# Performance work log

Measured on AMD Instinct MI355X. Metric: run time of the kernel, lower is better.

The kernel has to match this reference:

```python
import jax, jax.numpy as jnp
import numpy as np

N, E = 100000, 1600000
NFEAT, NHID, NCLASS, NLAYER = 128, 128, 40, 3


def _glorot(key, shape):
    fan_in, fan_out = shape[0], shape[1]
    lim = float(np.sqrt(6.0 / (fan_in + fan_out)))
    return jax.random.uniform(key, shape, jnp.float32, -lim, lim)


def setup_inputs() -> dict:
    key = jax.random.key(0)
    ks = jax.random.split(key, 12)
    x = jax.random.normal(ks[0], (N, NFEAT), jnp.float32)
    src = jax.random.randint(ks[1], (E,), 0, N, jnp.int32)
    dst = jax.random.randint(ks[2], (E,), 0, N, jnp.int32)
    W1 = _glorot(ks[3], (NFEAT, NHID)); b1 = jnp.zeros((NHID,), jnp.float32)
    W2 = _glorot(ks[4], (NHID, NHID)); b2 = jnp.zeros((NHID,), jnp.float32)
    Wg = jnp.stack([_glorot(ks[5 + l], (NHID, NHID)) for l in range(NLAYER)])  # [L,H,H]
    bg = jnp.zeros((NLAYER, NHID), jnp.float32)
    Wc = _glorot(ks[5 + NLAYER], (NHID, NCLASS)); bc = jnp.zeros((NCLASS,), jnp.float32)
    return {"x": x, "src": src, "dst": dst, "W1": W1, "b1": b1, "W2": W2,
            "b2": b2, "Wg": Wg, "bg": bg, "Wc": Wc, "bc": bc}


def _graph_conv(h, src, dst, W, b, out_norm, in_norm):
    # DGL GraphConv norm='both': scale by src out-deg^{-1/2}, sum-aggregate,
    # scale by dst in-deg^{-1/2}, then linear (in_feats == out_feats -> W after agg).
    h = h * out_norm[:, None]
    agg = jax.ops.segment_sum(h[src], dst, num_segments=N)
    return (agg * in_norm[:, None]) @ W + b


def reference(x, src, dst, W1, b1, W2, b2, Wg, bg, Wc, bc):
    ones = jnp.ones((E,), jnp.float32)
    out_deg = jnp.clip(jax.ops.segment_sum(ones, src, num_segments=N), 1.0)
    in_deg = jnp.clip(jax.ops.segment_sum(ones, dst, num_segments=N), 1.0)
    out_norm = jax.lax.rsqrt(out_deg)
    in_norm = jax.lax.rsqrt(in_deg)

    h = x @ W1 + b1            # feature1
    h = h @ W2 + b2            # feature2
    for l in range(NLAYER):    # stacked GraphConv + ReLU (dropout is identity in eval)
        h = _graph_conv(h, src, dst, Wg[l], bg[l], out_norm, in_norm)
        h = jax.nn.relu(h)
    return h @ Wc + bc         # classifier
```

## Files before the change

### kernel.cpp

```cpp
#include <hip/hip_runtime.h>
#include <hip/hip_fp16.h>
#include <cstdint>
#include <cstddef>

constexpr int NN  = 100000;
constexpr int EE  = 1600000;
constexpr int HID = 128;
constexpr int BUK = 256;
constexpr int NBUK = (NN + BUK - 1) / BUK;
constexpr int BLKE = 2048;
constexpr int NBE  = (EE + BLKE - 1) / BLKE;
constexpr int MH   = NBUK * NBE;
constexpr int MH2  = 2 * MH;
constexpr int NSC  = (MH2 + 2047) / 2048;

typedef float f32x4_t __attribute__((ext_vector_type(4)));
typedef short bf16x8_t __attribute__((ext_vector_type(8)));

static __device__ __forceinline__ short f2bf(float f) {
    union { float f; unsigned u; } x; x.f = f;
    unsigned r = x.u + 0x7FFF + ((x.u >> 16) & 1);
    return (short)(r >> 16);
}
static __device__ __forceinline__ float bf2f(short b) {
    union { unsigned u; float f; } x; x.u = ((unsigned)(unsigned short)b) << 16;
    return x.f;
}

__global__ __launch_bounds__(256) void bh_both_k(const int* __restrict__ src, const int* __restrict__ dst,
                                                 int* __restrict__ bh2) {
    __shared__ int hd[NBUK], hs[NBUK];
    int blk = blockIdx.x, t = threadIdx.x;
    for (int i = t; i < NBUK; i += 256) { hd[i] = 0; hs[i] = 0; }
    __syncthreads();
    int e0 = blk * BLKE, e1 = min(e0 + BLKE, EE);
    for (int e = e0 + t; e < e1; e += 256) {
        atomicAdd(&hd[dst[e] >> 8], 1);
        atomicAdd(&hs[src[e] >> 8], 1);
    }
    __syncthreads();
    for (int i = t; i < NBUK; i += 256) {
        bh2[i * NBE + blk]      = hd[i];
        bh2[MH + i * NBE + blk] = hs[i];
    }
}

__global__ __launch_bounds__(256) void scan_sum_k(const int* __restrict__ in, int* __restrict__ bsum, int n) {
    __shared__ int sc[256];
    int b = blockIdx.x, t = threadIdx.x;
    int base = b * 2048 + t * 8;
    int s = 0;
#pragma unroll
    for (int j = 0; j < 8; j++) { int idx = base + j; s += (idx < n) ? in[idx] : 0; }
    sc[t] = s; __syncthreads();
    for (int off = 128; off > 0; off >>= 1) {
        if (t < off) sc[t] += sc[t + off];
        __syncthreads();
    }
    if (t == 0) bsum[b] = sc[0];
}

__global__ __launch_bounds__(512) void scan_top_k(const int* __restrict__ bsum, int* __restrict__ boff, int nb) {
    __shared__ int sc[512];
    int t = threadIdx.x;
    int v = (t < nb) ? bsum[t] : 0;
    sc[t] = v; __syncthreads();
    for (int off = 1; off < 512; off <<= 1) {
        int u = (t >= off) ? sc[t - off] : 0;
        __syncthreads();
        sc[t] += u;
        __syncthreads();
    }
    if (t < nb) boff[t] = sc[t] - v;
}

__global__ __launch_bounds__(256) void scan_chunk_k(const int* __restrict__ in, const int* __restrict__ boff,
                                                    int* __restrict__ out, int n) {
    __shared__ int sc[256];
    int b = blockIdx.x, t = threadIdx.x;
    int base = b * 2048 + t * 8;
    int c[8];
    int s = 0;
#pragma unroll
    for (int j = 0; j < 8; j++) { int idx = base + j; c[j] = (idx < n) ? in[idx] : 0; s += c[j]; }
    sc[t] = s; __syncthreads();
    for (int off = 1; off < 256; off <<= 1) {
        int v = (t >= off) ? sc[t - off] : 0;
        __syncthreads();
        sc[t] += v;
        __syncthreads();
    }
    int excl = sc[t] - s + boff[b];
#pragma unroll
    for (int j = 0; j < 8; j++) {
        int idx = base + j;
        if (idx < n) out[idx] = excl;
        excl += c[j];
    }
}

__global__ __launch_bounds__(256) void scatter_both_k(const int* __restrict__ src, const int* __restrict__ dst,
                                                      const int* __restrict__ off2,
                                                      unsigned* __restrict__ pairs, unsigned char* __restrict__ sbyte) {
    __shared__ int cd[NBUK], cs[NBUK];
    int blk = blockIdx.x, t = threadIdx.x;
    for (int i = t; i < NBUK; i += 256) {
        cd[i] = off2[i * NBE + blk];
        cs[i] = off2[MH + i * NBE + blk] - EE;
    }
    __syncthreads();
    int e0 = blk * BLKE, e1 = min(e0 + BLKE, EE);
    for (int e = e0 + t; e < e1; e += 256) {
        int d = dst[e], s = src[e];
        int pd = atomicAdd(&cd[d >> 8], 1);
        pairs[pd] = ((unsigned)(d & 255) << 17) | (unsigned)s;
        int ps = atomicAdd(&cs[s >> 8], 1);
        sbyte[ps] = (unsigned char)(s & 255);
    }
}

__global__ __launch_bounds__(512) void bucket_csr_ocnt_k(
    const unsigned* __restrict__ pairs, const unsigned char* __restrict__ sbyte,
    const int* __restrict__ off2,
    int* __restrict__ rowptr, int* __restrict__ col,
    float* __restrict__ inorm, float* __restrict__ onorm) {
    __shared__ int hist[BUK];
    __shared__ int excl[BUK];
    __shared__ int psum[BUK];
    int t = threadIdx.x;

    if (blockIdx.x >= NBUK) {
        int b = blockIdx.x - NBUK;
        int base = off2[MH + b * NBE] - EE;
        int endv = (b == NBUK - 1) ? EE : off2[MH + (b + 1) * NBE] - EE;
        if (t < BUK) hist[t] = 0;
        __syncthreads();
        for (int i = base + t; i < endv; i += 512) atomicAdd(&hist[sbyte[i]], 1);
        __syncthreads();
        if (t < BUK) {
            int node = b * BUK + t;
            if (node < NN) {
                int c = hist[t]; if (c < 1) c = 1;
                onorm[node] = rsqrtf((float)c);
            }
        }
        return;
    }

    int b = blockIdx.x;
    int base = off2[b * NBE];
    int endv = (b == NBUK - 1) ? EE : off2[(b + 1) * NBE];
    if (t < BUK) hist[t] = 0;
    __syncthreads();
    for (int i = base + t; i < endv; i += 512) atomicAdd(&hist[pairs[i] >> 17], 1);
    __syncthreads();
    int ps = 0;
    if (t < BUK) { ps = hist[t]; psum[t] = ps; }
    __syncthreads();
    for (int off = 1; off < BUK; off <<= 1) {
        int u = 0;
        if (t < BUK && t >= off) u = psum[t - off];
        __syncthreads();
        if (t < BUK) psum[t] += u;
        __syncthreads();
    }
    if (t < BUK) {
        int pex = psum[t] - ps;
        excl[t] = pex;
        int node = b * BUK + t;
        if (node < NN) {
            rowptr[node] = base + pex;
            int c = ps; if (c < 1) c = 1;
            inorm[node] = rsqrtf((float)c);
        }
    }
    if (b == NBUK - 1 && t == 0) rowptr[NN] = EE;
    __syncthreads();
    for (int i = base + t; i < endv; i += 512) {
        unsigned p = pairs[i];
        int pos = base + atomicAdd(&excl[p >> 17], 1);
        col[pos] = (int)(p & 0x1FFFFu);
    }
}

__global__ __launch_bounds__(256) void w12_k(const float* __restrict__ W1, const float* __restrict__ W2,
                                             const float* __restrict__ b1, const float* __restrict__ b2,
                                             float* __restrict__ W12, float* __restrict__ b12) {
    if (blockIdx.x == 64) {
        int j = threadIdx.x;
        if (j < 128) {
            float acc = b2[j];
            for (int k = 0; k < 128; k++) acc = fmaf(b1[k], W2[k * 128 + j], acc);
            b12[j] = acc;
        }
        return;
    }
    int idx = blockIdx.x * 256 + threadIdx.x;
    int i = idx >> 7, j = idx & 127;
    float a0 = 0.f, a1 = 0.f, a2 = 0.f, a3 = 0.f;
    for (int k = 0; k < 128; k += 4) {
        a0 = fmaf(W1[i * 128 + k],     W2[(k)     * 128 + j], a0);
        a1 = fmaf(W1[i * 128 + k + 1], W2[(k + 1) * 128 + j], a1);
        a2 = fmaf(W1[i * 128 + k + 2], W2[(k + 2) * 128 + j], a2);
        a3 = fmaf(W1[i * 128 + k + 3], W2[(k + 3) * 128 + j], a3);
    }
    W12[idx] = (a0 + a1) + (a2 + a3);
}

__global__ __launch_bounds__(256) void agg_k(const float4* __restrict__ h16, const int* __restrict__ rowptr,
                                             const int* __restrict__ col, const float* __restrict__ inorm,
                                             short* __restrict__ h0h, short* __restrict__ h0l) {
    int w = (int)((blockIdx.x * 256 + threadIdx.x) >> 6);
    if (w >= NN) return;
    int lane = threadIdx.x & 63;
    int q   = lane >> 4;
    int l16 = lane & 15;
    int beg = rowptr[w], end = rowptr[w + 1];
    float acc[8];
#pragma unroll
    for (int j = 0; j < 8; j++) acc[j] = 0.f;

    union HU { float4 f4; __half2 h2[4]; };
    int i = beg + q;
    for (; i + 12 < end; i += 16) {
        int s0 = col[i], s1 = col[i + 4], s2 = col[i + 8], s3 = col[i + 12];
        HU u0, u1, u2, u3;
        u0.f4 = h16[(size_t)s0 * 16 + l16];
        u1.f4 = h16[(size_t)s1 * 16 + l16];
        u2.f4 = h16[(size_t)s2 * 16 + l16];
        u3.f4 = h16[(size_t)s3 * 16 + l16];
#pragma unroll
        for (int p = 0; p < 4; p++) {
            float2 a = __half22float2(u0.h2[p]);
            float2 b = __half22float2(u1.h2[p]);
            float2 c = __half22float2(u2.h2[p]);
            float2 d = __half22float2(u3.h2[p]);
            acc[2 * p]     += (a.x + b.x) + (c.x + d.x);
            acc[2 * p + 1] += (a.y + b.y) + (c.y + d.y);
        }
    }
    for (; i < end; i += 4) {
        int s = col[i];
        HU u; u.f4 = h16[(size_t)s * 16 + l16];
#pragma unroll
        for (int p = 0; p < 4; p++) {
            float2 a = __half22float2(u.h2[p]);
            acc[2 * p]     += a.x;
            acc[2 * p + 1] += a.y;
        }
    }
#pragma unroll
    for (int mm = 16; mm <= 32; mm <<= 1)
#pragma unroll
        for (int j = 0; j < 8; j++) acc[j] += __shfl_xor(acc[j], mm);
    if (q == 0) {
        float s = inorm[w];
        bf16x8_t hv, lv;
#pragma unroll
        for (int j = 0; j < 8; j++) {
            float v = acc[j] * s;
            short hi = f2bf(v);
            hv[j] = hi;
            lv[j] = f2bf(v - bf2f(hi));
        }
        *(bf16x8_t*)&h0h[(size_t)w * 128 + l16 * 8] = hv;
        *(bf16x8_t*)&h0l[(size_t)w * 128 + l16 * 8] = lv;
    }
}

template <int NT, bool RELU, bool OUTSCALE, bool OUTHALF, bool INSPLIT>
__global__ __launch_bounds__(256) void mfma_gemm_k(
    const void* __restrict__ in, const short* __restrict__ inl,
    const float* __restrict__ W, const float* __restrict__ bias,
    void* __restrict__ outp, const float* __restrict__ outscale,
    int nrows, int ncols, int ntiles) {

    __shared__ short Bh[NT * 2048];
    __shared__ short Bl[NT * 2048];
    __shared__ __half Tr[OUTHALF ? 4 * 16 * 128 : 1];

    const int t = threadIdx.x;

    if constexpr (NT == 8) {
        for (int j = 0; j < 16; j++) {
            int fi = (j * 256 + t) * 4;
            int k = fi >> 7, n0 = fi & 127;
            float4 wv = *(const float4*)(W + fi);
            float wa[4] = {wv.x, wv.y, wv.z, wv.w};
#pragma unroll
            for (int cc = 0; cc < 4; cc++) {
                int g = n0 + cc;
                int q2 = g >> 2;
                int ntc = q2 & 7;
                int c = ((q2 >> 3) << 2) | (g & 3);
                int kblk = k >> 5, ksub = k & 31;
                int lane_ = ((ksub >> 3) << 4) | c;
                int sidx = ((ntc * 4 + kblk) * 64 + lane_) * 8 + (ksub & 7);
                short hi = f2bf(wa[cc]);
                Bh[sidx] = hi; Bl[sidx] = f2bf(wa[cc] - bf2f(hi));
            }
        }
    } else {
        for (int idx = t; idx < 128 * 64; idx += 256) {
            int k = idx >> 6, g = idx & 63;
            if (g < NT * 16) {
                float w = (g < 40) ? ((const float*)W)[k * 40 + g] : 0.f;
                int q2 = g >> 2;
                int ntc = q2 % NT;
                int c = (q2 / NT) * 4 + (g & 3);
                int kblk = k >> 5, ksub = k & 31;
                int lane_ = ((ksub >> 3) << 4) | c;
                int sidx = ((ntc * 4 + kblk) * 64 + lane_) * 8 + (ksub & 7);
                short hi = f2bf(w);
                Bh[sidx] = hi; Bl[sidx] = f2bf(w - bf2f(hi));
            }
        }
    }
    __syncthreads();

    const int wave = t >> 6;
    const int lane = t & 63;
    const int m    = lane & 15;
    const int kq   = lane >> 4;
    const int cbase = kq * 4 * NT;

    float bstat[4 * NT];
#pragma unroll
    for (int i = 0; i < 4 * NT; i++) {
        int g = cbase + i;
        bstat[i] = (g < ncols) ? bias[g] : 0.f;
    }

    const int wstride = gridDim.x * 4;
    for (int tile = blockIdx.x * 4 + wave; tile < ntiles; tile += wstride) {
        int row = tile * 16 + m;
        bool rv = row < nrows;

        bf16x8_t Ah[4], Al[4];
        if constexpr (INSPLIT) {
            const short* ih = (const short*)in + (size_t)row * 128 + kq * 8;
            const short* il = inl + (size_t)row * 128 + kq * 8;
#pragma unroll
            for (int kb = 0; kb < 4; kb++) {
                if (rv) {
                    Ah[kb] = *(const bf16x8_t*)(ih + kb * 32);
                    Al[kb] = *(const bf16x8_t*)(il + kb * 32);
                } else {
                    Ah[kb] = (bf16x8_t){0,0,0,0,0,0,0,0};
                    Al[kb] = (bf16x8_t){0,0,0,0,0,0,0,0};
                }
            }
        } else {
#pragma unroll
            for (int kb = 0; kb < 4; kb++) {
                const float* ap = (const float*)in + (size_t)row * 128 + kb * 32 + kq * 8;
                float4 p0, p1;
                if (rv) { p0 = *(const float4*)ap; p1 = *(const float4*)(ap + 4); }
                else    { p0 = make_float4(0,0,0,0); p1 = make_float4(0,0,0,0); }
                float av[8] = {p0.x, p0.y, p0.z, p0.w, p1.x, p1.y, p1.z, p1.w};
#pragma unroll
                for (int j = 0; j < 8; j++) {
                    float v = av[j];
                    short hi = f2bf(v);
                    Ah[kb][j] = hi;
                    Al[kb][j] = f2bf(v - bf2f(hi));
                }
            }
        }

        float osc = 1.f;
        if (OUTSCALE && rv) osc = outscale[row];

        float ov[4 * NT] __attribute__((aligned(16)));
#pragma unroll
        for (int nt = 0; nt < NT; nt++) {
            f32x4_t acc = {0.f, 0.f, 0.f, 0.f};
#pragma unroll
            for (int kb = 0; kb < 4; kb++) {
                const bf16x8_t bh = *(const bf16x8_t*)&Bh[((nt * 4 + kb) * 64 + lane) * 8];
                const bf16x8_t bl = *(const bf16x8_t*)&Bl[((nt * 4 + kb) * 64 + lane) * 8];
                acc = __builtin_amdgcn_mfma_f32_16x16x32_bf16(bh, Ah[kb], acc, 0, 0, 0);
                acc = __builtin_amdgcn_mfma_f32_16x16x32_bf16(bh, Al[kb], acc, 0, 0, 0);
                acc = __builtin_amdgcn_mfma_f32_16x16x32_bf16(bl, Ah[kb], acc, 0, 0, 0);
            }
#pragma unroll
            for (int r = 0; r < 4; r++) {
                float v = acc[r] + bstat[nt * 4 + r];
                if (RELU) v = fmaxf(v, 0.f);
                ov[nt * 4 + r] = v * osc;
            }
        }

        if constexpr (OUTHALF) {
            __half* tw = &Tr[wave * 2048];
#pragma unroll
            for (int p = 0; p < 4; p++) {
                union { __half h[8]; float4 f4; } U;
#pragma unroll
                for (int j = 0; j < 8; j++) U.h[j] = __float2half_rn(ov[p * 8 + j]);
                int bo = (cbase * 2 + p * 16) ^ ((m & 7) << 4);
                *(float4*)((char*)(tw + m * 128) + bo) = U.f4;
            }
#pragma unroll
            for (int s2 = 0; s2 < 4; s2++) {
                int r = s2 * 4 + (lane >> 4);
                int bo = ((lane & 15) * 16) ^ ((r & 7) << 4);
                float4 v = *(const float4*)((char*)(tw + r * 128) + bo);
                *(float4*)((__half*)outp + (size_t)(tile * 16 + r) * ncols + (lane & 15) * 8) = v;
            }
        } else if (rv) {
            if constexpr (NT == 8) {
                float4* p = (float4*)((float*)outp + (size_t)row * 128 + cbase);
#pragma unroll
                for (int j = 0; j < 8; j++) p[j] = ((const float4*)ov)[j];
            } else {
                float* p = (float*)outp + (size_t)row * 40 + cbase;
#pragma unroll
                for (int j = 0; j < 3; j++) {
                    if (cbase + j * 4 < 40) *(float4*)(p + j * 4) = ((const float4*)ov)[j];
                }
            }
        }
    }
}

extern "C" void kernel_launch(void* const* d_in, const int* in_sizes, int n_in,
                              void* d_out, int out_size, void* d_ws, size_t ws_size,
                              hipStream_t stream) {
    const float* x   = (const float*)d_in[0];
    const int*   src = (const int*)d_in[1];
    const int*   dst = (const int*)d_in[2];
    const float* W1  = (const float*)d_in[3];
    const float* b1  = (const float*)d_in[4];
    const float* W2  = (const float*)d_in[5];
    const float* b2  = (const float*)d_in[6];
    const float* Wg  = (const float*)d_in[7];
    const float* bg  = (const float*)d_in[8];
    const float* Wc  = (const float*)d_in[9];
    const float* bc  = (const float*)d_in[10];
    float* out = (float*)d_out;

    char* ws = (char*)d_ws;
    size_t off = 0;
    auto alloc = [&](size_t bytes) -> void* {
        void* p = ws + off;
        off += (bytes + 255) & ~(size_t)255;
        return p;
    };
    short*  h0h    = (short*)alloc((size_t)NN * HID * 2);
    short*  h0l    = (short*)alloc((size_t)NN * HID * 2);
    float*  h1     = (float*)alloc((size_t)NN * HID * 4);
    __half* h16    = (__half*)alloc((size_t)NN * HID * 2);
    float*  W12    = (float*)alloc(128 * 128 * 4);
    float*  b12    = (float*)alloc(128 * 4);
    float*  onorm  = (float*)alloc((size_t)NN * 4);
    float*  inorm  = (float*)alloc((size_t)NN * 4);
    int*    rowptr = (int*)alloc((size_t)(NN + 1) * 4);
    int*    col    = (int*)alloc((size_t)EE * 4);
    int*    bh2    = (int*)alloc((size_t)MH2 * 4);
    int*    off2   = (int*)alloc((size_t)MH2 * 4);
    int*    bsum   = (int*)alloc((size_t)NSC * 4);
    int*    boff   = (int*)alloc((size_t)NSC * 4);
    unsigned*      pairs = (unsigned*)h0h;
    unsigned char* sbyte = (unsigned char*)h0h + (size_t)EE * 4;

    bh_both_k<<<NBE, 256, 0, stream>>>(src, dst, bh2);
    scan_sum_k<<<NSC, 256, 0, stream>>>(bh2, bsum, MH2);
    scan_top_k<<<1, 512, 0, stream>>>(bsum, boff, NSC);
    scan_chunk_k<<<NSC, 256, 0, stream>>>(bh2, boff, off2, MH2);
    scatter_both_k<<<NBE, 256, 0, stream>>>(src, dst, off2, pairs, sbyte);
    bucket_csr_ocnt_k<<<2 * NBUK, 512, 0, stream>>>(pairs, sbyte, off2,
                                                    rowptr, col, inorm, onorm);

    w12_k<<<65, 256, 0, stream>>>(W1, W2, b1, b2, W12, b12);

    const int ntiles = NN / 16;
    const int ggrid  = 512;

    mfma_gemm_k<8, false, true, true, false><<<ggrid, 256, 0, stream>>>(
        x, nullptr, W12, b12, h16, onorm, NN, 128, ntiles);
    for (int l = 0; l < 3; l++) {
        agg_k<<<(NN * 64 + 255) / 256, 256, 0, stream>>>(
            (const float4*)h16, rowptr, col, inorm, h0h, h0l);
        if (l < 2) {
            mfma_gemm_k<8, true, true, true, true><<<ggrid, 256, 0, stream>>>(
                h0h, h0l, Wg + (size_t)l * 128 * 128, bg + (size_t)l * 128, h16, onorm, NN, 128, ntiles);
        } else {
            mfma_gemm_k<8, true, false, false, true><<<ggrid, 256, 0, stream>>>(
                h0h, h0l, Wg + (size_t)l * 128 * 128, bg + (size_t)l * 128, h1, nullptr, NN, 128, ntiles);
        }
    }
    mfma_gemm_k<3, false, false, false, false><<<ggrid, 256, 0, stream>>>(
        h1, nullptr, Wc, bc, out, nullptr, NN, 40, ntiles);
}
```

Baseline: 552.9 us.

## Pre-stage split bf16 weights in global memory and read B fragments directly

A new kernel converts W12 and the three GraphConv weight matrices into hi/lo bf16 MFMA-fragment layout once, storing them in workspace. The 128-wide GEMMs no longer build that layout in shared memory per block and instead load B fragments from global memory (expected to hit in cache). The grid is raised to 1563 blocks so each wave handles roughly one tile. This removes per-block conversion work and frees LDS for occupancy, at the cost of repeated global/L2 fragment loads inside the MFMA loop.

```diff
diff --git a/kernel.cpp b/kernel.cpp
--- a/kernel.cpp
+++ b/kernel.cpp
@@ -207,6 +207,33 @@
     W12[idx] = (a0 + a1) + (a2 + a3);
 }
 
+__global__ __launch_bounds__(256) void stage_w_k(const float* __restrict__ W12, const float* __restrict__ Wg,
+                                                 short* __restrict__ wsp) {
+    int mat = blockIdx.x;
+    const float* W = (mat == 0) ? W12 : (Wg + (size_t)(mat - 1) * 128 * 128);
+    short* Bh = wsp + (size_t)mat * 2 * 16384;
+    short* Bl = Bh + 16384;
+    int t = threadIdx.x;
+    for (int j = 0; j < 16; j++) {
+        int fi = (j * 256 + t) * 4;
+        int k = fi >> 7, n0 = fi & 127;
+        float4 wv = *(const float4*)(W + fi);
+        float wa[4] = {wv.x, wv.y, wv.z, wv.w};
+#pragma unroll
+        for (int cc = 0; cc < 4; cc++) {
+            int g = n0 + cc;
+            int q2 = g >> 2;
+            int ntc = q2 & 7;
+            int c = ((q2 >> 3) << 2) | (g & 3);
+            int kblk = k >> 5, ksub = k & 31;
+            int lane_ = ((ksub >> 3) << 4) | c;
+            int sidx = ((ntc * 4 + kblk) * 64 + lane_) * 8 + (ksub & 7);
+            short hi = f2bf(wa[cc]);
+            Bh[sidx] = hi; Bl[sidx] = f2bf(wa[cc] - bf2f(hi));
+        }
+    }
+}
+
 __global__ __launch_bounds__(256) void agg_k(const float4* __restrict__ h16, const int* __restrict__ rowptr,
                                              const int* __restrict__ col, const float* __restrict__ inorm,
                                              short* __restrict__ h0h, short* __restrict__ h0l) {
@@ -268,65 +295,26 @@
     }
 }
 
-template <int NT, bool RELU, bool OUTSCALE, bool OUTHALF, bool INSPLIT>
-__global__ __launch_bounds__(256) void mfma_gemm_k(
+template <bool RELU, bool OUTSCALE, bool OUTHALF, bool INSPLIT>
+__global__ __launch_bounds__(256) void gw_gemm_k(
     const void* __restrict__ in, const short* __restrict__ inl,
-    const float* __restrict__ W, const float* __restrict__ bias,
+    const short* __restrict__ gBh, const short* __restrict__ gBl,
+    const float* __restrict__ bias,
     void* __restrict__ outp, const float* __restrict__ outscale,
     int nrows, int ncols, int ntiles) {
 
-    __shared__ short Bh[NT * 2048];
-    __shared__ short Bl[NT * 2048];
     __shared__ __half Tr[OUTHALF ? 4 * 16 * 128 : 1];
 
     const int t = threadIdx.x;
-
-    if constexpr (NT == 8) {
-        for (int j = 0; j < 16; j++) {
-            int fi = (j * 256 + t) * 4;
-            int k = fi >> 7, n0 = fi & 127;
-            float4 wv = *(const float4*)(W + fi);
-            float wa[4] = {wv.x, wv.y, wv.z, wv.w};
-#pragma unroll
-            for (int cc = 0; cc < 4; cc++) {
-                int g = n0 + cc;
-                int q2 = g >> 2;
-                int ntc = q2 & 7;
-                int c = ((q2 >> 3) << 2) | (g & 3);
-                int kblk = k >> 5, ksub = k & 31;
-                int lane_ = ((ksub >> 3) << 4) | c;
-                int sidx = ((ntc * 4 + kblk) * 64 + lane_) * 8 + (ksub & 7);
-                short hi = f2bf(wa[cc]);
-                Bh[sidx] = hi; Bl[sidx] = f2bf(wa[cc] - bf2f(hi));
-            }
-        }
-    } else {
-        for (int idx = t; idx < 128 * 64; idx += 256) {
-            int k = idx >> 6, g = idx & 63;
-            if (g < NT * 16) {
-                float w = (g < 40) ? ((const float*)W)[k * 40 + g] : 0.f;
-                int q2 = g >> 2;
-                int ntc = q2 % NT;
-                int c = (q2 / NT) * 4 + (g & 3);
-                int kblk = k >> 5, ksub = k & 31;
-                int lane_ = ((ksub >> 3) << 4) | c;
-                int sidx = ((ntc * 4 + kblk) * 64 + lane_) * 8 + (ksub & 7);
-                short hi = f2bf(w);
-                Bh[sidx] = hi; Bl[sidx] = f2bf(w - bf2f(hi));
-            }
-        }
-    }
-    __syncthreads();
-
     const int wave = t >> 6;
     const int lane = t & 63;
     const int m    = lane & 15;
     const int kq   = lane >> 4;
-    const int cbase = kq * 4 * NT;
-
-    float bstat[4 * NT];
-#pragma unroll
-    for (int i = 0; i < 4 * NT; i++) {
+    const int cbase = kq * 32;
+
+    float bstat[32];
+#pragma unroll
+    for (int i = 0; i < 32; i++) {
         int g = cbase + i;
         bstat[i] = (g < ncols) ? bias[g] : 0.f;
     }
@@ -371,6 +359,114 @@
         float osc = 1.f;
         if (OUTSCALE && rv) osc = outscale[row];
 
+        float ov[32] __attribute__((aligned(16)));
+#pragma unroll
+        for (int nt = 0; nt < 8; nt++) {
+            f32x4_t acc = {0.f, 0.f, 0.f, 0.f};
+#pragma unroll
+            for (int kb = 0; kb < 4; kb++) {
+                const bf16x8_t bh = *(const bf16x8_t*)&gBh[((nt * 4 + kb) * 64 + lane) * 8];
+                const bf16x8_t bl = *(const bf16x8_t*)&gBl[((nt * 4 + kb) * 64 + lane) * 8];
+                acc = __builtin_amdgcn_mfma_f32_16x16x32_bf16(bh, Ah[kb], acc, 0, 0, 0);
+                acc = __builtin_amdgcn_mfma_f32_16x16x32_bf16(bh, Al[kb], acc, 0, 0, 0);
+                acc = __builtin_amdgcn_mfma_f32_16x16x32_bf16(bl, Ah[kb], acc, 0, 0, 0);
+            }
+#pragma unroll
+            for (int r = 0; r < 4; r++) {
+                float v = acc[r] + bstat[nt * 4 + r];
+                if (RELU) v = fmaxf(v, 0.f);
+                ov[nt * 4 + r] = v * osc;
+            }
+        }
+
+        if constexpr (OUTHALF) {
+            __half* tw = &Tr[wave * 2048];
+#pragma unroll
+            for (int p = 0; p < 4; p++) {
+                union { __half h[8]; float4 f4; } U;
+#pragma unroll
+                for (int j = 0; j < 8; j++) U.h[j] = __float2half_rn(ov[p * 8 + j]);
+                int bo = (cbase * 2 + p * 16) ^ ((m & 7) << 4);
+                *(float4*)((char*)(tw + m * 128) + bo) = U.f4;
+            }
+#pragma unroll
+            for (int s2 = 0; s2 < 4; s2++) {
+                int r = s2 * 4 + (lane >> 4);
+                int bo = ((lane & 15) * 16) ^ ((r & 7) << 4);
+                float4 v = *(const float4*)((char*)(tw + r * 128) + bo);
+                *(float4*)((__half*)outp + (size_t)(tile * 16 + r) * ncols + (lane & 15) * 8) = v;
+            }
+        } else if (rv) {
+            float4* p = (float4*)((float*)outp + (size_t)row * 128 + cbase);
+#pragma unroll
+            for (int j = 0; j < 8; j++) p[j] = ((const float4*)ov)[j];
+        }
+    }
+}
+
+template <int NT, bool RELU, bool OUTSCALE, bool OUTHALF, bool INSPLIT>
+__global__ __launch_bounds__(256) void mfma_gemm_k(
+    const void* __restrict__ in, const short* __restrict__ inl,
+    const float* __restrict__ W, const float* __restrict__ bias,
+    void* __restrict__ outp, const float* __restrict__ outscale,
+    int nrows, int ncols, int ntiles) {
+
+    __shared__ short Bh[NT * 2048];
+    __shared__ short Bl[NT * 2048];
+
+    const int t = threadIdx.x;
+
+    for (int idx = t; idx < 128 * 64; idx += 256) {
+        int k = idx >> 6, g = idx & 63;
+        if (g < NT * 16) {
+            float w = (g < 40) ? ((const float*)W)[k * 40 + g] : 0.f;
+            int q2 = g >> 2;
+            int ntc = q2 % NT;
+            int c = (q2 / NT) * 4 + (g & 3);
+            int kblk = k >> 5, ksub = k & 31;
+            int lane_ = ((ksub >> 3) << 4) | c;
+            int sidx = ((ntc * 4 + kblk) * 64 + lane_) * 8 + (ksub & 7);
+            short hi = f2bf(w);
+            Bh[sidx] = hi; Bl[sidx] = f2bf(w - bf2f(hi));
+        }
+    }
+    __syncthreads();
+
+    const int wave = t >> 6;
+    const int lane = t & 63;
+    const int m    = lane & 15;
+    const int kq   = lane >> 4;
+    const int cbase = kq * 4 * NT;
+
+    float bstat[4 * NT];
+#pragma unroll
+    for (int i = 0; i < 4 * NT; i++) {
+        int g = cbase + i;
+        bstat[i] = (g < ncols) ? bias[g] : 0.f;
+    }
+
+    const int wstride = gridDim.x * 4;
+    for (int tile = blockIdx.x * 4 + wave; tile < ntiles; tile += wstride) {
+        int row = tile * 16 + m;
+        bool rv = row < nrows;
+
+        bf16x8_t Ah[4], Al[4];
+#pragma unroll
+        for (int kb = 0; kb < 4; kb++) {
+            const float* ap = (const float*)in + (size_t)row * 128 + kb * 32 + kq * 8;
+            float4 p0, p1;
+            if (rv) { p0 = *(const float4*)ap; p1 = *(const float4*)(ap + 4); }
+            else    { p0 = make_float4(0,0,0,0); p1 = make_float4(0,0,0,0); }
+            float av[8] = {p0.x, p0.y, p0.z, p0.w, p1.x, p1.y, p1.z, p1.w};
+#pragma unroll
+            for (int j = 0; j < 8; j++) {
+                float v = av[j];
+                short hi = f2bf(v);
+                Ah[kb][j] = hi;
+                Al[kb][j] = f2bf(v - bf2f(hi));
+            }
+        }
+
         float ov[4 * NT] __attribute__((aligned(16)));
 #pragma unroll
         for (int nt = 0; nt < NT; nt++) {
@@ -384,41 +480,14 @@
                 acc = __builtin_amdgcn_mfma_f32_16x16x32_bf16(bl, Ah[kb], acc, 0, 0, 0);
             }
 #pragma unroll
-            for (int r = 0; r < 4; r++) {
-                float v = acc[r] + bstat[nt * 4 + r];
-                if (RELU) v = fmaxf(v, 0.f);
-                ov[nt * 4 + r] = v * osc;
-            }
-        }
-
-        if constexpr (OUTHALF) {
-            __half* tw = &Tr[wave * 2048];
-#pragma unroll
-            for (int p = 0; p < 4; p++) {
-                union { __half h[8]; float4 f4; } U;
-#pragma unroll
-                for (int j = 0; j < 8; j++) U.h[j] = __float2half_rn(ov[p * 8 + j]);
-                int bo = (cbase * 2 + p * 16) ^ ((m & 7) << 4);
-                *(float4*)((char*)(tw + m * 128) + bo) = U.f4;
-            }
-#pragma unroll
-            for (int s2 = 0; s2 < 4; s2++) {
-                int r = s2 * 4 + (lane >> 4);
-                int bo = ((lane & 15) * 16) ^ ((r & 7) << 4);
-                float4 v = *(const float4*)((char*)(tw + r * 128) + bo);
-                *(float4*)((__half*)outp + (size_t)(tile * 16 + r) * ncols + (lane & 15) * 8) = v;
-            }
-        } else if (rv) {
-            if constexpr (NT == 8) {
-                float4* p = (float4*)((float*)outp + (size_t)row * 128 + cbase);
-#pragma unroll
-                for (int j = 0; j < 8; j++) p[j] = ((const float4*)ov)[j];
-            } else {
-                float* p = (float*)outp + (size_t)row * 40 + cbase;
-#pragma unroll
-                for (int j = 0; j < 3; j++) {
-                    if (cbase + j * 4 < 40) *(float4*)(p + j * 4) = ((const float4*)ov)[j];
-                }
+            for (int r = 0; r < 4; r++) ov[nt * 4 + r] = acc[r] + bstat[nt * 4 + r];
+        }
+
+        if (rv) {
+            float* p = (float*)outp + (size_t)row * 40 + cbase;
+#pragma unroll
+            for (int j = 0; j < 3; j++) {
+                if (cbase + j * 4 < 40) *(float4*)(p + j * 4) = ((const float4*)ov)[j];
             }
         }
     }
@@ -453,6 +522,7 @@
     __half* h16    = (__half*)alloc((size_t)NN * HID * 2);
     float*  W12    = (float*)alloc(128 * 128 * 4);
     float*  b12    = (float*)alloc(128 * 4);
+    short*  wsp    = (short*)alloc(4 * 2 * 16384 * 2);
     float*  onorm  = (float*)alloc((size_t)NN * 4);
     float*  inorm  = (float*)alloc((size_t)NN * 4);
     int*    rowptr = (int*)alloc((size_t)(NN + 1) * 4);
@@ -473,23 +543,31 @@
                                                     rowptr, col, inorm, onorm);
 
     w12_k<<<65, 256, 0, stream>>>(W1, W2, b1, b2, W12, b12);
+    stage_w_k<<<4, 256, 0, stream>>>(W12, Wg, wsp);
 
     const int ntiles = NN / 16;
-    const int ggrid  = 512;
-
-    mfma_gemm_k<8, false, true, true, false><<<ggrid, 256, 0, stream>>>(
-        x, nullptr, W12, b12, h16, onorm, NN, 128, ntiles);
+    const int ggrid  = 1563;
+
+    const short* pW12h = wsp;                const short* pW12l = wsp + 16384;
+    const short* pWg0h = wsp + 1 * 32768;    const short* pWg0l = pWg0h + 16384;
+    const short* pWg1h = wsp + 2 * 32768;    const short* pWg1l = pWg1h + 16384;
+    const short* pWg2h = wsp + 3 * 32768;    const short* pWg2l = pWg2h + 16384;
+
+    gw_gemm_k<false, true, true, false><<<ggrid, 256, 0, stream>>>(
+        x, nullptr, pW12h, pW12l, b12, h16, onorm, NN, 128, ntiles);
     for (int l = 0; l < 3; l++) {
         agg_k<<<(NN * 64 + 255) / 256, 256, 0, stream>>>(
             (const float4*)h16, rowptr, col, inorm, h0h, h0l);
+        const short* ph = (l == 0) ? pWg0h : (l == 1) ? pWg1h : pWg2h;
+        const short* pl = (l == 0) ? pWg0l : (l == 1) ? pWg1l : pWg2l;
         if (l < 2) {
-            mfma_gemm_k<8, true, true, true, true><<<ggrid, 256, 0, stream>>>(
-                h0h, h0l, Wg + (size_t)l * 128 * 128, bg + (size_t)l * 128, h16, onorm, NN, 128, ntiles);
+            gw_gemm_k<true, true, true, true><<<ggrid, 256, 0, stream>>>(
+                h0h, h0l, ph, pl, bg + (size_t)l * 128, h16, onorm, NN, 128, ntiles);
         } else {
-            mfma_gemm_k<8, true, false, false, true><<<ggrid, 256, 0, stream>>>(
-                h0h, h0l, Wg + (size_t)l * 128 * 128, bg + (size_t)l * 128, h1, nullptr, NN, 128, ntiles);
-        }
-    }
-    mfma_gemm_k<3, false, false, false, false><<<ggrid, 256, 0, stream>>>(
+            gw_gemm_k<true, false, false, true><<<ggrid, 256, 0, stream>>>(
+                h0h, h0l, ph, pl, bg + (size_t)l * 128, h1, nullptr, NN, 128, ntiles);
+        }
+    }
+    mfma_gemm_k<3, false, false, false, false><<<512, 256, 0, stream>>>(
         h1, nullptr, Wc, bc, out, nullptr, NN, 40, ntiles);
 }
```

Measured after the change: 575.9 us. 4.2% more time.

## Fuse last GraphConv GEMM with classifier GEMM, pre-swizzle final layer weights

Applied to the files above, without the earlier changes.

Replaces the last layer's GEMM plus separate classifier GEMM with one kernel that computes ReLU(h·Wg2+b) per tile, stages the result as split bf16 hi/lo in shared memory, and immediately applies Wc. This removes the fp32 h1 intermediate write and read (about 51 MB each way) and one kernel launch. Wg2 is pre-swizzled into the MFMA B-fragment layout by an extra block in the weight-prep kernel, and the fused kernel reads that fragment directly from global memory in its inner loop. The added cost is more registers and shared memory per block, plus a per-block Wc swizzle into shared memory.

```diff
diff --git a/kernel.cpp b/kernel.cpp
--- a/kernel.cpp
+++ b/kernel.cpp
@@ -185,9 +185,36 @@
 
 __global__ __launch_bounds__(256) void w12_k(const float* __restrict__ W1, const float* __restrict__ W2,
                                              const float* __restrict__ b1, const float* __restrict__ b2,
-                                             float* __restrict__ W12, float* __restrict__ b12) {
+                                             const float* __restrict__ Wg,
+                                             float* __restrict__ W12, float* __restrict__ b12,
+                                             short* __restrict__ wsp) {
+    int t = threadIdx.x;
+    if (blockIdx.x == 65) {
+        const float* W = Wg + 2 * 128 * 128;
+        short* Bh = wsp;
+        short* Bl = wsp + 16384;
+        for (int j = 0; j < 16; j++) {
+            int fi = (j * 256 + t) * 4;
+            int k = fi >> 7, n0 = fi & 127;
+            float4 wv = *(const float4*)(W + fi);
+            float wa[4] = {wv.x, wv.y, wv.z, wv.w};
+#pragma unroll
+            for (int cc = 0; cc < 4; cc++) {
+                int g = n0 + cc;
+                int q2 = g >> 2;
+                int ntc = q2 & 7;
+                int c = ((q2 >> 3) << 2) | (g & 3);
+                int kblk = k >> 5, ksub = k & 31;
+                int lane_ = ((ksub >> 3) << 4) | c;
+                int sidx = ((ntc * 4 + kblk) * 64 + lane_) * 8 + (ksub & 7);
+                short hi = f2bf(wa[cc]);
+                Bh[sidx] = hi; Bl[sidx] = f2bf(wa[cc] - bf2f(hi));
+            }
+        }
+        return;
+    }
     if (blockIdx.x == 64) {
-        int j = threadIdx.x;
+        int j = t;
         if (j < 128) {
             float acc = b2[j];
             for (int k = 0; k < 128; k++) acc = fmaf(b1[k], W2[k * 128 + j], acc);
@@ -195,7 +222,7 @@
         }
         return;
     }
-    int idx = blockIdx.x * 256 + threadIdx.x;
+    int idx = blockIdx.x * 256 + t;
     int i = idx >> 7, j = idx & 127;
     float a0 = 0.f, a1 = 0.f, a2 = 0.f, a3 = 0.f;
     for (int k = 0; k < 128; k += 4) {
@@ -420,6 +447,127 @@
                     if (cbase + j * 4 < 40) *(float4*)(p + j * 4) = ((const float4*)ov)[j];
                 }
             }
+        }
+    }
+}
+
+__global__ __launch_bounds__(256) void conv_cls_k(
+    const short* __restrict__ inh, const short* __restrict__ inl,
+    const short* __restrict__ gBh, const short* __restrict__ gBl,
+    const float* __restrict__ bg2,
+    const float* __restrict__ Wc, const float* __restrict__ bc,
+    float* __restrict__ out, int ntiles) {
+
+    __shared__ short WcH[3 * 2048];
+    __shared__ short WcL[3 * 2048];
+    __shared__ short Lh[4][16][136];
+    __shared__ short Ll[4][16][136];
+
+    const int t = threadIdx.x;
+
+    for (int idx = t; idx < 128 * 64; idx += 256) {
+        int k = idx >> 6, g = idx & 63;
+        if (g < 48) {
+            float w = (g < 40) ? Wc[k * 40 + g] : 0.f;
+            int q2 = g >> 2;
+            int ntc = q2 % 3;
+            int c = (q2 / 3) * 4 + (g & 3);
+            int kblk = k >> 5, ksub = k & 31;
+            int lane_ = ((ksub >> 3) << 4) | c;
+            int sidx = ((ntc * 4 + kblk) * 64 + lane_) * 8 + (ksub & 7);
+            short hi = f2bf(w);
+            WcH[sidx] = hi; WcL[sidx] = f2bf(w - bf2f(hi));
+        }
+    }
+    __syncthreads();
+
+    const int wave = t >> 6;
+    const int lane = t & 63;
+    const int m    = lane & 15;
+    const int kq   = lane >> 4;
+    const int cbase = kq * 32;
+    const int cbc   = kq * 12;
+
+    float bstat[32];
+#pragma unroll
+    for (int i = 0; i < 32; i++) bstat[i] = bg2[cbase + i];
+    float bstatC[12];
+#pragma unroll
+    for (int i = 0; i < 12; i++) {
+        int g = cbc + i;
+        bstatC[i] = (g < 40) ? bc[g] : 0.f;
+    }
+
+    const int wstride = gridDim.x * 4;
+    for (int tile = blockIdx.x * 4 + wave; tile < ntiles; tile += wstride) {
+        const int row = tile * 16 + m;
+
+        bf16x8_t Ah[4], Al[4];
+        {
+            const short* ih = inh + (size_t)row * 128 + kq * 8;
+            const short* il = inl + (size_t)row * 128 + kq * 8;
+#pragma unroll
+            for (int kb = 0; kb < 4; kb++) {
+                Ah[kb] = *(const bf16x8_t*)(ih + kb * 32);
+                Al[kb] = *(const bf16x8_t*)(il + kb * 32);
+            }
+        }
+
+        float ov[32] __attribute__((aligned(16)));
+#pragma unroll
+        for (int nt = 0; nt < 8; nt++) {
+            f32x4_t acc = {0.f, 0.f, 0.f, 0.f};
+#pragma unroll
+            for (int kb = 0; kb < 4; kb++) {
+                const bf16x8_t bh = *(const bf16x8_t*)&gBh[((nt * 4 + kb) * 64 + lane) * 8];
+                const bf16x8_t bl = *(const bf16x8_t*)&gBl[((nt * 4 + kb) * 64 + lane) * 8];
+                acc = __builtin_amdgcn_mfma_f32_16x16x32_bf16(bh, Ah[kb], acc, 0, 0, 0);
+                acc = __builtin_amdgcn_mfma_f32_16x16x32_bf16(bh, Al[kb], acc, 0, 0, 0);
+                acc = __builtin_amdgcn_mfma_f32_16x16x32_bf16(bl, Ah[kb], acc, 0, 0, 0);
+            }
+#pragma unroll
+            for (int r = 0; r < 4; r++) {
+                float v = acc[r] + bstat[nt * 4 + r];
+                ov[nt * 4 + r] = fmaxf(v, 0.f);
+            }
+        }
+
+#pragma unroll
+        for (int p = 0; p < 4; p++) {
+            bf16x8_t hv, lv;
+#pragma unroll
+            for (int j = 0; j < 8; j++) {
+                float v = ov[p * 8 + j];
+                short hi = f2bf(v);
+                hv[j] = hi;
+                lv[j] = f2bf(v - bf2f(hi));
+            }
+            *(bf16x8_t*)&Lh[wave][m][cbase + p * 8] = hv;
+            *(bf16x8_t*)&Ll[wave][m][cbase + p * 8] = lv;
+        }
+
+        float ovc[12] __attribute__((aligned(16)));
+#pragma unroll
+        for (int ntc = 0; ntc < 3; ntc++) {
+            f32x4_t acc = {0.f, 0.f, 0.f, 0.f};
+#pragma unroll
+            for (int kb = 0; kb < 4; kb++) {
+                const bf16x8_t wh = *(const bf16x8_t*)&WcH[((ntc * 4 + kb) * 64 + lane) * 8];
+                const bf16x8_t wl = *(const bf16x8_t*)&WcL[((ntc * 4 + kb) * 64 + lane) * 8];
+                const bf16x8_t fh = *(const bf16x8_t*)&Lh[wave][m][kb * 32 + kq * 8];
+                const bf16x8_t fl = *(const bf16x8_t*)&Ll[wave][m][kb * 32 + kq * 8];
+                acc = __builtin_amdgcn_mfma_f32_16x16x32_bf16(wh, fh, acc, 0, 0, 0);
+                acc = __builtin_amdgcn_mfma_f32_16x16x32_bf16(wh, fl, acc, 0, 0, 0);
+                acc = __builtin_amdgcn_mfma_f32_16x16x32_bf16(wl, fh, acc, 0, 0, 0);
+            }
+#pragma unroll
+            for (int r = 0; r < 4; r++) ovc[ntc * 4 + r] = acc[r] + bstatC[ntc * 4 + r];
+        }
+
+        float* p = out + (size_t)row * 40 + cbc;
+#pragma unroll
+        for (int j = 0; j < 3; j++) {
+            if (cbc + j * 4 < 40) *(float4*)(p + j * 4) = ((const float4*)ovc)[j];
         }
     }
 }
@@ -449,10 +597,10 @@
     };
     short*  h0h    = (short*)alloc((size_t)NN * HID * 2);
     short*  h0l    = (short*)alloc((size_t)NN * HID * 2);
-    float*  h1     = (float*)alloc((size_t)NN * HID * 4);
     __half* h16    = (__half*)alloc((size_t)NN * HID * 2);
     float*  W12    = (float*)alloc(128 * 128 * 4);
     float*  b12    = (float*)alloc(128 * 4);
+    short*  wsp    = (short*)alloc(2 * 16384 * 2);
     float*  onorm  = (float*)alloc((size_t)NN * 4);
     float*  inorm  = (float*)alloc((size_t)NN * 4);
     int*    rowptr = (int*)alloc((size_t)(NN + 1) * 4);
@@ -472,7 +620,7 @@
     bucket_csr_ocnt_k<<<2 * NBUK, 512, 0, stream>>>(pairs, sbyte, off2,
                                                     rowptr, col, inorm, onorm);
 
-    w12_k<<<65, 256, 0, stream>>>(W1, W2, b1, b2, W12, b12);
+    w12_k<<<66, 256, 0, stream>>>(W1, W2, b1, b2, Wg, W12, b12, wsp);
 
     const int ntiles = NN / 16;
     const int ggrid  = 512;
@@ -486,10 +634,8 @@
             mfma_gemm_k<8, true, true, true, true><<<ggrid, 256, 0, stream>>>(
                 h0h, h0l, Wg + (size_t)l * 128 * 128, bg + (size_t)l * 128, h16, onorm, NN, 128, ntiles);
         } else {
-            mfma_gemm_k<8, true, false, false, true><<<ggrid, 256, 0, stream>>>(
-                h0h, h0l, Wg + (size_t)l * 128 * 128, bg + (size_t)l * 128, h1, nullptr, NN, 128, ntiles);
-        }
-    }
-    mfma_gemm_k<3, false, false, false, false><<<ggrid, 256, 0, stream>>>(
-        h1, nullptr, Wc, bc, out, nullptr, NN, 40, ntiles);
-}
+            conv_cls_k<<<ggrid, 256, 0, stream>>>(
+                h0h, h0l, wsp, wsp + 16384, bg + 2 * 128, Wc, bc, out, ntiles);
+        }
+    }
+}
```

After: 534.7 us. 1.03x faster.
